# Kernel tuning notes

Measured on AMD Instinct MI355X. Metric: run time of the kernel, lower is better.

The kernel has to match this reference:

```python
import jax, jax.numpy as jnp
import numpy as np

D_MODEL = 1024
N_HEAD = 16
HEAD_DIM = D_MODEL // N_HEAD
D_FF = int(D_MODEL * 4.0)
B, T = 2, 2048


def rms_norm(x, eps=1e-6):
    return x * jax.lax.rsqrt(jnp.mean(jnp.square(x), axis=-1, keepdims=True) + eps)


def rope_tables(T, head_dim):
    # half-truncated RoPE: first quarter of dims get real freqs, next quarter zeros
    angular_freq = (1.0 / 1024.0) ** jnp.linspace(0.0, 1.0, head_dim // 4, dtype=jnp.float32)
    angular_freq = jnp.concatenate([angular_freq, jnp.zeros(head_dim // 4, jnp.float32)])
    theta = jnp.arange(T, dtype=jnp.float32)[:, None] * angular_freq[None, :]  # [T, head_dim//2]
    return jnp.cos(theta), jnp.sin(theta)


def apply_rope(x, cos, sin):
    # x: [B, H, T, D]; cos/sin: [T, D//2]
    x1, x2 = jnp.split(x.astype(jnp.float32), 2, axis=-1)
    c = cos[None, None]
    s = sin[None, None]
    y1 = x1 * c + x2 * s
    y2 = -x1 * s + x2 * c
    return jnp.concatenate([y1, y2], axis=-1).astype(x.dtype)


def setup_inputs() -> dict:
    key = jax.random.key(0)
    ks = jax.random.split(key, 10)
    x = jax.random.normal(ks[0], (B, T, D_MODEL), jnp.float32)
    block_mask = jnp.tril(jnp.ones((T, T), jnp.bool_))  # causal
    sc = 1.0 / np.sqrt(D_MODEL)
    Wqkv = jax.random.normal(ks[1], (D_MODEL, 3 * D_MODEL), jnp.float32) * sc
    bqkv = jnp.zeros((3 * D_MODEL,), jnp.float32)
    Wo = jax.random.normal(ks[2], (D_MODEL, D_MODEL), jnp.float32) * sc
    bo = jnp.zeros((D_MODEL,), jnp.float32)
    W1 = jax.random.normal(ks[3], (D_MODEL, D_FF), jnp.float32) * sc
    b1 = jnp.zeros((D_FF,), jnp.float32)
    W2 = jax.random.normal(ks[4], (D_FF, D_MODEL), jnp.float32) * (1.0 / np.sqrt(D_FF))
    b2 = jnp.zeros((D_MODEL,), jnp.float32)
    return {"x": x, "block_mask": block_mask, "Wqkv": Wqkv, "bqkv": bqkv,
            "Wo": Wo, "bo": bo, "W1": W1, "b1": b1, "W2": W2, "b2": b2}


def reference(x, block_mask, Wqkv, bqkv, Wo, bo, W1, b1, W2, b2):
    Bq, Tq, D = x.shape
    cos, sin = rope_tables(Tq, HEAD_DIM)

    def attn(h):
        qkv = h @ Wqkv + bqkv  # [B, T, 3D]
        qkv = qkv.reshape(Bq, Tq, 3, N_HEAD, HEAD_DIM)
        qkv = jnp.transpose(qkv, (2, 0, 3, 1, 4))  # [3, B, H, T, d]
        q, k, v = qkv[0], qkv[1], qkv[2]
        q, k = rms_norm(q), rms_norm(k)
        q, k = apply_rope(q, cos, sin), apply_rope(k, cos, sin)
        scores = jnp.einsum('bhtd,bhsd->bhts', q, k) / np.sqrt(HEAD_DIM)
        scores = jnp.where(block_mask[None, None], scores, jnp.float32(-1e30))
        p = jax.nn.softmax(scores, axis=-1)
        o = jnp.einsum('bhts,bhsd->bhtd', p, v)
        o = jnp.transpose(o, (0, 2, 1, 3)).reshape(Bq, Tq, D)
        return o @ Wo + bo

    def mlp(h):
        return jax.nn.gelu(h @ W1 + b1) @ W2 + b2

    x = x + attn(rms_norm(x))
    x = x + mlp(rms_norm(x))
    return x
```

## Files before the change

kernel.cpp:

```cpp
#include <hip/hip_runtime.h>
#include <hip/hip_bf16.h>


typedef __attribute__((ext_vector_type(8))) short short8;
typedef __attribute__((ext_vector_type(4))) float f32x4;
typedef __attribute__((ext_vector_type(8))) unsigned short u16x8;

#define MROWS 4096
#define DMODEL 1024
#define DFF 4096
#define NH 16
#define HD 64
#define SEQ 2048

static __device__ __forceinline__ unsigned short f2bf(float f) {
    union { __hip_bfloat16 b; unsigned short u; } cv;
    cv.b = __float2bfloat16(f);
    return cv.u;
}

static __device__ __forceinline__ void gload_lds16(const void* g, void* l) {
    __builtin_amdgcn_global_load_lds(
        (const __attribute__((address_space(1))) unsigned int*)g,
        (__attribute__((address_space(3))) unsigned int*)l, 16, 0, 0);
}

static __device__ __forceinline__ int xcd_swizzle(int id, int nwg) {
    const int nx = 8;
    const int q = nwg / nx, r = nwg % nx;
    const int xcd = id % nx, loc = id / nx;
    return (xcd < r ? xcd * (q + 1) : r * (q + 1) + (xcd - r) * q) + loc;
}

__global__ void cast_transpose(const float* __restrict__ W,
                               unsigned short* __restrict__ Wt, int K, int N) {
    __shared__ float tile[32][33];
    const int tx = threadIdx.x & 31;
    const int ty = threadIdx.x >> 5;
    const int n0 = blockIdx.x * 32, k0 = blockIdx.y * 32;
#pragma unroll
    for (int i = 0; i < 4; ++i) {
        int kk = ty + i * 8;
        tile[kk][tx] = W[(long)(k0 + kk) * N + n0 + tx];
    }
    __syncthreads();
#pragma unroll
    for (int i = 0; i < 4; ++i) {
        int nn = ty + i * 8;
        Wt[(long)(n0 + nn) * K + k0 + tx] = f2bf(tile[tx][nn]);
    }
}

__global__ void rope_table(float* __restrict__ cosT, float* __restrict__ sinT) {
    const int t = blockIdx.x, j = threadIdx.x;
    float th = (j < 16) ? (float)t * exp2f(-(10.0f / 15.0f) * (float)j) : 0.0f;
    cosT[t * 32 + j] = cosf(th);
    sinT[t * 32 + j] = sinf(th);
}

__global__ void rmsnorm_cast(const float* __restrict__ xin,
                             unsigned short* __restrict__ hout) {
    const int row = blockIdx.x;
    const float4 v = ((const float4*)(xin + (long)row * DMODEL))[threadIdx.x];
    float ss = v.x * v.x + v.y * v.y + v.z * v.z + v.w * v.w;
#pragma unroll
    for (int m = 32; m >= 1; m >>= 1) ss += __shfl_xor(ss, m);
    __shared__ float part[4];
    if ((threadIdx.x & 63) == 0) part[threadIdx.x >> 6] = ss;
    __syncthreads();
    const float tot = part[0] + part[1] + part[2] + part[3];
    const float sc = rsqrtf(tot * (1.0f / (float)DMODEL) + 1e-6f);
    ushort4 o;
    o.x = f2bf(v.x * sc); o.y = f2bf(v.y * sc);
    o.z = f2bf(v.z * sc); o.w = f2bf(v.w * sc);
    ((ushort4*)hout)[(long)row * (DMODEL / 4) + threadIdx.x] = o;
}

template <int EPI>
__launch_bounds__(256)
__global__ void gemm_bt(const short* __restrict__ A, const short* __restrict__ Bt,
                        const float* __restrict__ bias, const float* __restrict__ res,
                        float* __restrict__ outF, unsigned short* __restrict__ outB,
                        int N, int K) {
    __shared__ short As[3][128 * 32];
    __shared__ short Bs[3][128 * 32];
    const int tid = threadIdx.x;
    const int lane = tid & 63, w = tid >> 6;
    const int wr = w >> 1, wc = w & 1;
    const int l16 = lane & 15, lhi = lane >> 4;

    const int nwg = gridDim.x * gridDim.y;
    int id = xcd_swizzle(blockIdx.y * gridDim.x + blockIdx.x, nwg);
    const int bx = id % gridDim.x, by = id / gridDim.x;
    const long rowA0 = (long)by * 128;
    const long rowB0 = (long)bx * 128;

    const f32x4 fz = {0.f, 0.f, 0.f, 0.f};
    f32x4 acc[4][4];
#pragma unroll
    for (int m = 0; m < 4; ++m)
#pragma unroll
        for (int n = 0; n < 4; ++n) acc[m][n] = fz;

    auto stage = [&](int kt, int b) {
        const int k0 = kt << 5;
#pragma unroll
        for (int it = 0; it < 2; ++it) {
            const int c = it * 256 + w * 64 + lane;
            const int r = c >> 2, col = (c & 3) << 3;
            gload_lds16(A + (rowA0 + r) * K + k0 + col, (char*)As[b] + c * 16);
            gload_lds16(Bt + (rowB0 + r) * K + k0 + col, (char*)Bs[b] + c * 16);
        }
    };
    auto compute = [&](int b) {
        short8 af[4], bf[4];
#pragma unroll
        for (int m = 0; m < 4; ++m)
            af[m] = *(const short8*)(&As[b][0] + (wr * 64 + m * 16 + l16) * 32 + lhi * 8);
#pragma unroll
        for (int n = 0; n < 4; ++n)
            bf[n] = *(const short8*)(&Bs[b][0] + (wc * 64 + n * 16 + l16) * 32 + lhi * 8);
#pragma unroll
        for (int m = 0; m < 4; ++m)
#pragma unroll
            for (int n = 0; n < 4; ++n)
                acc[m][n] = __builtin_amdgcn_mfma_f32_16x16x32_bf16(
                    af[m], bf[n], acc[m][n], 0, 0, 0);
    };

    const int ktiles = K >> 5;
    stage(0, 0);
    if (ktiles > 1) {
        stage(1, 1);
        asm volatile("s_waitcnt vmcnt(4)" ::: "memory");
    } else {
        asm volatile("s_waitcnt vmcnt(0)" ::: "memory");
    }
    __builtin_amdgcn_s_barrier();
    __builtin_amdgcn_sched_barrier(0);

    int b0 = 0, b1 = 1, b2 = 2;
    for (int kt = 0; kt < ktiles; ++kt) {
        if (kt + 2 < ktiles) stage(kt + 2, b2);
        compute(b0);
        if (kt + 1 < ktiles) {
            if (kt + 2 < ktiles) asm volatile("s_waitcnt vmcnt(4)" ::: "memory");
            else                 asm volatile("s_waitcnt vmcnt(0)" ::: "memory");
            __builtin_amdgcn_s_barrier();
            __builtin_amdgcn_sched_barrier(0);
        }
        const int t = b0; b0 = b1; b1 = b2; b2 = t;
    }

#pragma unroll
    for (int m = 0; m < 4; ++m) {
        const long r0 = rowA0 + wr * 64 + m * 16 + lhi * 4;
#pragma unroll
        for (int n = 0; n < 4; ++n) {
            const long cc = rowB0 + wc * 64 + n * 16 + l16;
            const float bv = bias[cc];
#pragma unroll
            for (int j = 0; j < 4; ++j) {
                const long idx = (r0 + j) * N + cc;
                float v = acc[m][n][j] + bv;
                if (EPI == 1) v += res[idx];
                if (EPI == 2) {
                    float g = 0.5f * v *
                        (1.0f + tanhf(0.7978845608028654f * (v + 0.044715f * v * v * v)));
                    outB[idx] = f2bf(g);
                } else {
                    outF[idx] = v;
                }
            }
        }
    }
}

__global__ void qkv_post(const float* __restrict__ qkv, const float* __restrict__ cosT,
                         const float* __restrict__ sinT, unsigned short* __restrict__ Qo,
                         unsigned short* __restrict__ Ko) {
    const int lane = threadIdx.x & 63;
    const int g = blockIdx.x * 4 + (threadIdx.x >> 6);
    const int row = g >> 4, h = g & 15;
    const int b = row >> 11, t = row & 2047;
    const float* base = qkv + (long)row * 3072 + h * 64;
    float q = base[lane];
    float k = base[1024 + lane];
    float sq = q * q, sk = k * k;
#pragma unroll
    for (int m = 32; m >= 1; m >>= 1) {
        sq += __shfl_xor(sq, m);
        sk += __shfl_xor(sk, m);
    }
    q *= rsqrtf(sq * (1.0f / 64.0f) + 1e-6f);
    k *= rsqrtf(sk * (1.0f / 64.0f) + 1e-6f);
    const int j = lane & 31;
    const float c = cosT[t * 32 + j], s = sinT[t * 32 + j];
    const float q2 = __shfl_xor(q, 32), k2 = __shfl_xor(k, 32);
    const float sgn = (lane < 32) ? 1.0f : -1.0f;
    const float qr = q * c + sgn * q2 * s;
    const float kr = k * c + sgn * k2 * s;
    const long o = ((long)(b * 16 + h) * SEQ + t) * 64 + lane;
    Qo[o] = f2bf(qr * 0.125f);
    Ko[o] = f2bf(kr);
}

__global__ void transpose_v(const float* __restrict__ qkv,
                            unsigned short* __restrict__ Vt) {
    __shared__ float tile[64][65];
    const int tid = threadIdx.x;
    const int bh = blockIdx.x, tt = blockIdx.y;
    const int b = bh >> 4, h = bh & 15;
    const int tr = tid >> 2, c0 = (tid & 3) * 16;
    const float* src = qkv + ((long)(b * SEQ + tt * 64 + tr)) * 3072 + 2048 + h * 64 + c0;
#pragma unroll
    for (int i = 0; i < 4; ++i) {
        float4 v = ((const float4*)src)[i];
        tile[tr][c0 + i * 4 + 0] = v.x;
        tile[tr][c0 + i * 4 + 1] = v.y;
        tile[tr][c0 + i * 4 + 2] = v.z;
        tile[tr][c0 + i * 4 + 3] = v.w;
    }
    __syncthreads();
    const int d = tid >> 2, t0 = (tid & 3) * 16;
    unsigned short* dst = Vt + ((long)bh * 64 + d) * SEQ + tt * 64 + t0;
#pragma unroll
    for (int half = 0; half < 2; ++half) {
        u16x8 o;
#pragma unroll
        for (int e = 0; e < 8; ++e) o[e] = f2bf(tile[t0 + half * 8 + e][d]);
        *(u16x8*)(dst + half * 8) = o;
    }
}

__launch_bounds__(256)
__global__ void attn_fwd(const short* __restrict__ Qg, const short* __restrict__ Kg,
                         const short* __restrict__ Vtg, unsigned short* __restrict__ Og) {
    __shared__ short Ks[64 * 64];
    __shared__ short Vs[64 * 64];
    __shared__ char Ps[4][16 * 128];
    const int tid = threadIdx.x, lane = tid & 63, w = tid >> 6;
    const int l16 = lane & 15, lhi = lane >> 4;
    int id = xcd_swizzle(blockIdx.y * gridDim.x + blockIdx.x, 1024);
    const int bh = id >> 5;
    const int qt = 31 - (id & 31);
    const int bb = bh >> 4, hh = bh & 15;
    const long base_q = (long)bh * (SEQ * 64);

    short8 aq0, aq1;
    {
        const short* Qp = Qg + base_q + (long)(qt * 64 + w * 16) * 64;
        aq0 = *(const short8*)(Qp + l16 * 64 + lhi * 8);
        aq1 = *(const short8*)(Qp + l16 * 64 + 32 + lhi * 8);
    }
    float mrow[4] = {-1e30f, -1e30f, -1e30f, -1e30f};
    float lrow[4] = {0.f, 0.f, 0.f, 0.f};
    const f32x4 fz = {0.f, 0.f, 0.f, 0.f};
    f32x4 oacc[4];
#pragma unroll
    for (int n = 0; n < 4; ++n) oacc[n] = fz;

    char* Pw = &Ps[w][0];

    for (int kt = 0; kt <= qt; ++kt) {
        const short* Kp = Kg + base_q + (long)kt * 64 * 64;
        const short* Vp = Vtg + base_q + (long)kt * 64;
#pragma unroll
        for (int it = 0; it < 2; ++it) {
            const int c = it * 256 + w * 64 + lane;
            const int r = c >> 3;
            const int col = ((c & 7) ^ (r & 7)) << 3;
            gload_lds16(Kp + r * 64 + col, (char*)Ks + c * 16);
            gload_lds16(Vp + (long)r * SEQ + col, (char*)Vs + c * 16);
        }
        __syncthreads();

        f32x4 s[4];
        __builtin_amdgcn_s_setprio(1);
#pragma unroll
        for (int n = 0; n < 4; ++n) {
            const int kr = n * 16 + l16;
            short8 bk0 = *(const short8*)(Ks + kr * 64 + ((lhi ^ (kr & 7)) << 3));
            short8 bk1 = *(const short8*)(Ks + kr * 64 + (((lhi + 4) ^ (kr & 7)) << 3));
            f32x4 z = fz;
            z = __builtin_amdgcn_mfma_f32_16x16x32_bf16(aq0, bk0, z, 0, 0, 0);
            s[n] = __builtin_amdgcn_mfma_f32_16x16x32_bf16(aq1, bk1, z, 0, 0, 0);
        }
        __builtin_amdgcn_s_setprio(0);
        if (kt == qt) {
#pragma unroll
            for (int n = 0; n < 4; ++n)
#pragma unroll
                for (int j = 0; j < 4; ++j)
                    if (n * 16 + l16 > w * 16 + lhi * 4 + j) s[n][j] = -1e30f;
        }

#pragma unroll
        for (int j = 0; j < 4; ++j) {
            float pm = fmaxf(fmaxf(s[0][j], s[1][j]), fmaxf(s[2][j], s[3][j]));
            pm = fmaxf(pm, __shfl_xor(pm, 1));
            pm = fmaxf(pm, __shfl_xor(pm, 2));
            pm = fmaxf(pm, __shfl_xor(pm, 4));
            pm = fmaxf(pm, __shfl_xor(pm, 8));
            const float newm = fmaxf(mrow[j], pm);
            const float sc = __expf(mrow[j] - newm);
            float ps = 0.f;
#pragma unroll
            for (int n = 0; n < 4; ++n) {
                float p = __expf(s[n][j] - newm);
                s[n][j] = p;
                ps += p;
            }
            ps += __shfl_xor(ps, 1);
            ps += __shfl_xor(ps, 2);
            ps += __shfl_xor(ps, 4);
            ps += __shfl_xor(ps, 8);
            lrow[j] = lrow[j] * sc + ps;
            mrow[j] = newm;
#pragma unroll
            for (int n = 0; n < 4; ++n) oacc[n][j] *= sc;
        }

#pragma unroll
        for (int n = 0; n < 4; ++n)
#pragma unroll
            for (int j = 0; j < 4; ++j) {
                const int q = lhi * 4 + j, colp = n * 16 + l16;
                *(short*)(Pw + ((q * 128 + colp * 2) ^ ((q & 7) << 4))) =
                    (short)f2bf(s[n][j]);
            }
        __builtin_amdgcn_s_setprio(1);
#pragma unroll
        for (int ks = 0; ks < 2; ++ks) {
            short8 pa = *(const short8*)(Pw + ((l16 * 128 + ks * 64 + lhi * 16) ^ ((l16 & 7) << 4)));
#pragma unroll
            for (int n = 0; n < 4; ++n) {
                const int dr = n * 16 + l16;
                short8 vb = *(const short8*)(Vs + dr * 64 + ((((ks << 2) + lhi) ^ (dr & 7)) << 3));
                oacc[n] = __builtin_amdgcn_mfma_f32_16x16x32_bf16(pa, vb, oacc[n], 0, 0, 0);
            }
        }
        __builtin_amdgcn_s_setprio(0);
        __syncthreads();
    }

#pragma unroll
    for (int n = 0; n < 4; ++n)
#pragma unroll
        for (int j = 0; j < 4; ++j) {
            const int qrow = qt * 64 + w * 16 + lhi * 4 + j;
            const long orow = (long)bb * SEQ + qrow;
            const int col = hh * 64 + n * 16 + l16;
            Og[orow * DMODEL + col] = f2bf(oacc[n][j] / lrow[j]);
        }
}

extern "C" void kernel_launch(void* const* d_in, const int* in_sizes, int n_in,
                              void* d_out, int out_size, void* d_ws, size_t ws_size,
                              hipStream_t stream) {
    const float* x    = (const float*)d_in[0];
    const float* Wqkv = (const float*)d_in[2];
    const float* bqkv = (const float*)d_in[3];
    const float* Wo   = (const float*)d_in[4];
    const float* bo   = (const float*)d_in[5];
    const float* W1   = (const float*)d_in[6];
    const float* b1   = (const float*)d_in[7];
    const float* W2   = (const float*)d_in[8];
    const float* b2   = (const float*)d_in[9];
    float* out = (float*)d_out;

    char* ws = (char*)d_ws;
    auto alloc = [&](size_t b) {
        char* p = ws;
        ws += (b + 255) & ~(size_t)255;
        return p;
    };
    short* WqkvT = (short*)alloc(3072ull * 1024 * 2);
    short* WoT   = (short*)alloc(1024ull * 1024 * 2);
    short* W1T   = (short*)alloc(4096ull * 1024 * 2);
    short* W2T   = (short*)alloc(1024ull * 4096 * 2);
    float* cosT  = (float*)alloc(2048ull * 32 * 4);
    float* sinT  = (float*)alloc(2048ull * 32 * 4);
    short* hbuf  = (short*)alloc((size_t)MROWS * DMODEL * 2);
    short* Qb    = (short*)alloc(32ull * SEQ * 64 * 2);
    short* Kb    = (short*)alloc(32ull * SEQ * 64 * 2);
    short* Vtb   = (short*)alloc(32ull * 64 * SEQ * 2);
    short* Ob    = (short*)alloc((size_t)MROWS * DMODEL * 2);
    float* x1    = (float*)alloc((size_t)MROWS * DMODEL * 4);
    char*  big   = alloc((size_t)MROWS * 3072 * 4);
    float* qkv   = (float*)big;
    unsigned short* act = (unsigned short*)big;

    cast_transpose<<<dim3(96, 32), 256, 0, stream>>>(Wqkv, (unsigned short*)WqkvT, 1024, 3072);
    cast_transpose<<<dim3(32, 32), 256, 0, stream>>>(Wo, (unsigned short*)WoT, 1024, 1024);
    cast_transpose<<<dim3(128, 32), 256, 0, stream>>>(W1, (unsigned short*)W1T, 1024, 4096);
    cast_transpose<<<dim3(32, 128), 256, 0, stream>>>(W2, (unsigned short*)W2T, 4096, 1024);
    rope_table<<<2048, 32, 0, stream>>>(cosT, sinT);
    rmsnorm_cast<<<MROWS, 256, 0, stream>>>(x, (unsigned short*)hbuf);
    gemm_bt<0><<<dim3(24, 32), 256, 0, stream>>>(hbuf, WqkvT, bqkv, nullptr, qkv, nullptr, 3072, 1024);
    qkv_post<<<16384, 256, 0, stream>>>(qkv, cosT, sinT,
                                        (unsigned short*)Qb, (unsigned short*)Kb);
    transpose_v<<<dim3(32, 32), 256, 0, stream>>>(qkv, (unsigned short*)Vtb);
    attn_fwd<<<dim3(32, 32), 256, 0, stream>>>(Qb, Kb, Vtb, (unsigned short*)Ob);
    gemm_bt<1><<<dim3(8, 32), 256, 0, stream>>>(Ob, WoT, bo, x, x1, nullptr, 1024, 1024);
    rmsnorm_cast<<<MROWS, 256, 0, stream>>>(x1, (unsigned short*)hbuf);
    gemm_bt<2><<<dim3(32, 32), 256, 0, stream>>>(hbuf, W1T, b1, nullptr, nullptr, act, 4096, 1024);
    gemm_bt<1><<<dim3(8, 32), 256, 0, stream>>>((const short*)act, W2T, b2, x1, out, nullptr, 1024, 4096);
}
```

Baseline: 464.1 us.

## Template GEMM on N-tile width and switch to double-buffered pipeline

```diff
diff --git a/kernel.cpp b/kernel.cpp
--- a/kernel.cpp
+++ b/kernel.cpp
@@ -76,14 +76,15 @@
     ((ushort4*)hout)[(long)row * (DMODEL / 4) + threadIdx.x] = o;
 }
 
-template <int EPI>
+template <int EPI, int BN>
 __launch_bounds__(256)
 __global__ void gemm_bt(const short* __restrict__ A, const short* __restrict__ Bt,
                         const float* __restrict__ bias, const float* __restrict__ res,
                         float* __restrict__ outF, unsigned short* __restrict__ outB,
                         int N, int K) {
-    __shared__ short As[3][128 * 32];
-    __shared__ short Bs[3][128 * 32];
+    constexpr int NF = BN / 32;
+    __shared__ short As[2][128 * 32];
+    __shared__ short Bs[2][BN * 32];
     const int tid = threadIdx.x;
     const int lane = tid & 63, w = tid >> 6;
     const int wr = w >> 1, wc = w & 1;
@@ -93,71 +94,63 @@
     int id = xcd_swizzle(blockIdx.y * gridDim.x + blockIdx.x, nwg);
     const int bx = id % gridDim.x, by = id / gridDim.x;
     const long rowA0 = (long)by * 128;
-    const long rowB0 = (long)bx * 128;
+    const long rowB0 = (long)bx * BN;
 
     const f32x4 fz = {0.f, 0.f, 0.f, 0.f};
-    f32x4 acc[4][4];
+    f32x4 acc[4][NF];
 #pragma unroll
     for (int m = 0; m < 4; ++m)
 #pragma unroll
-        for (int n = 0; n < 4; ++n) acc[m][n] = fz;
+        for (int n = 0; n < NF; ++n) acc[m][n] = fz;
 
     auto stage = [&](int kt, int b) {
         const int k0 = kt << 5;
 #pragma unroll
         for (int it = 0; it < 2; ++it) {
-            const int c = it * 256 + w * 64 + lane;
+            const int c = it * 256 + tid;
             const int r = c >> 2, col = (c & 3) << 3;
             gload_lds16(A + (rowA0 + r) * K + k0 + col, (char*)As[b] + c * 16);
+        }
+#pragma unroll
+        for (int it = 0; it < BN / 64; ++it) {
+            const int c = it * 256 + tid;
+            const int r = c >> 2, col = (c & 3) << 3;
             gload_lds16(Bt + (rowB0 + r) * K + k0 + col, (char*)Bs[b] + c * 16);
         }
     };
     auto compute = [&](int b) {
-        short8 af[4], bf[4];
+        short8 af[4], bf[NF];
 #pragma unroll
         for (int m = 0; m < 4; ++m)
             af[m] = *(const short8*)(&As[b][0] + (wr * 64 + m * 16 + l16) * 32 + lhi * 8);
 #pragma unroll
-        for (int n = 0; n < 4; ++n)
-            bf[n] = *(const short8*)(&Bs[b][0] + (wc * 64 + n * 16 + l16) * 32 + lhi * 8);
+        for (int n = 0; n < NF; ++n)
+            bf[n] = *(const short8*)(&Bs[b][0] + (wc * (BN / 2) + n * 16 + l16) * 32 + lhi * 8);
 #pragma unroll
         for (int m = 0; m < 4; ++m)
 #pragma unroll
-            for (int n = 0; n < 4; ++n)
+            for (int n = 0; n < NF; ++n)
                 acc[m][n] = __builtin_amdgcn_mfma_f32_16x16x32_bf16(
                     af[m], bf[n], acc[m][n], 0, 0, 0);
     };
 
     const int ktiles = K >> 5;
     stage(0, 0);
-    if (ktiles > 1) {
-        stage(1, 1);
-        asm volatile("s_waitcnt vmcnt(4)" ::: "memory");
-    } else {
-        asm volatile("s_waitcnt vmcnt(0)" ::: "memory");
-    }
-    __builtin_amdgcn_s_barrier();
-    __builtin_amdgcn_sched_barrier(0);
-
-    int b0 = 0, b1 = 1, b2 = 2;
+    __syncthreads();
+    int cur = 0;
     for (int kt = 0; kt < ktiles; ++kt) {
-        if (kt + 2 < ktiles) stage(kt + 2, b2);
-        compute(b0);
-        if (kt + 1 < ktiles) {
-            if (kt + 2 < ktiles) asm volatile("s_waitcnt vmcnt(4)" ::: "memory");
-            else                 asm volatile("s_waitcnt vmcnt(0)" ::: "memory");
-            __builtin_amdgcn_s_barrier();
-            __builtin_amdgcn_sched_barrier(0);
-        }
-        const int t = b0; b0 = b1; b1 = b2; b2 = t;
+        if (kt + 1 < ktiles) stage(kt + 1, cur ^ 1);
+        compute(cur);
+        __syncthreads();
+        cur ^= 1;
     }
 
 #pragma unroll
     for (int m = 0; m < 4; ++m) {
         const long r0 = rowA0 + wr * 64 + m * 16 + lhi * 4;
 #pragma unroll
-        for (int n = 0; n < 4; ++n) {
-            const long cc = rowB0 + wc * 64 + n * 16 + l16;
+        for (int n = 0; n < NF; ++n) {
+            const long cc = rowB0 + wc * (BN / 2) + n * 16 + l16;
             const float bv = bias[cc];
 #pragma unroll
             for (int j = 0; j < 4; ++j) {
@@ -397,13 +390,13 @@
     cast_transpose<<<dim3(32, 128), 256, 0, stream>>>(W2, (unsigned short*)W2T, 4096, 1024);
     rope_table<<<2048, 32, 0, stream>>>(cosT, sinT);
     rmsnorm_cast<<<MROWS, 256, 0, stream>>>(x, (unsigned short*)hbuf);
-    gemm_bt<0><<<dim3(24, 32), 256, 0, stream>>>(hbuf, WqkvT, bqkv, nullptr, qkv, nullptr, 3072, 1024);
+    gemm_bt<0, 128><<<dim3(24, 32), 256, 0, stream>>>(hbuf, WqkvT, bqkv, nullptr, qkv, nullptr, 3072, 1024);
     qkv_post<<<16384, 256, 0, stream>>>(qkv, cosT, sinT,
                                         (unsigned short*)Qb, (unsigned short*)Kb);
     transpose_v<<<dim3(32, 32), 256, 0, stream>>>(qkv, (unsigned short*)Vtb);
     attn_fwd<<<dim3(32, 32), 256, 0, stream>>>(Qb, Kb, Vtb, (unsigned short*)Ob);
-    gemm_bt<1><<<dim3(8, 32), 256, 0, stream>>>(Ob, WoT, bo, x, x1, nullptr, 1024, 1024);
+    gemm_bt<1, 64><<<dim3(16, 32), 256, 0, stream>>>(Ob, WoT, bo, x, x1, nullptr, 1024, 1024);
     rmsnorm_cast<<<MROWS, 256, 0, stream>>>(x1, (unsigned short*)hbuf);
-    gemm_bt<2><<<dim3(32, 32), 256, 0, stream>>>(hbuf, W1T, b1, nullptr, nullptr, act, 4096, 1024);
-    gemm_bt<1><<<dim3(8, 32), 256, 0, stream>>>((const short*)act, W2T, b2, x1, out, nullptr, 1024, 4096);
-}
+    gemm_bt<2, 128><<<dim3(32, 32), 256, 0, stream>>>(hbuf, W1T, b1, nullptr, nullptr, act, 4096, 1024);
+    gemm_bt<1, 64><<<dim3(16, 32), 256, 0, stream>>>((const short*)act, W2T, b2, x1, out, nullptr, 1024, 4096);
+}
```

Measured after the change: 447.8 us. -3.5%, faster.
